# Performance work log

Hardware: AMD Instinct MI355X
Metric: run time of the kernel (lower is better)

Reference implementation:

```python
import jax, jax.numpy as jnp
import numpy as np

N_NODES = 64
KS = (52, 42, 34)  # ceil(0.8*64), ceil(0.8*52), ceil(0.8*42)


def _gcn(x, A, W, b):
    # GCNConv(improved=True): self-loop fill 2.0, symmetric normalization. A[tgt, src], weighted.
    n = A.shape[0]
    Ah = A + 2.0 * jnp.eye(n, dtype=A.dtype)
    d = Ah.sum(-1)
    dis = jnp.where(d > 0, jax.lax.rsqrt(d), 0.0)
    An = dis[:, None] * Ah * dis[None, :]
    return An @ (x @ W) + b


def _augment(A):
    # GraphUNet.augment_adj: add self loops (weight 1), A2 = A1 @ A1, remove self loops
    n = A.shape[0]
    eye = jnp.eye(n, dtype=A.dtype)
    A1 = A + eye
    return (A1 @ A1) * (1.0 - eye)


def _pool(x, A, w, k):
    # TopKPooling: score = tanh(x.w/||w||), keep top-k, scale kept features by score
    s = jnp.tanh((x @ w) / jnp.linalg.norm(w))
    sv, perm = jax.lax.top_k(s, k)
    return x[perm] * sv[:, None], A[perm][:, perm], perm


def _unet(x, A, dw0, db0, dws, dbs, pws, uws, ubs, uwl, ubl):
    # GraphUNet(depth=3, sum_res=True), single graph: x [n, F2], A [n, n]
    x = jax.nn.relu(_gcn(x, A, dw0, db0))
    xs, As, perms = [x], [A], []
    for i in range(3):
        A = _augment(A)
        x, A, perm = _pool(x, A, pws[i], KS[i])
        x = jax.nn.relu(_gcn(x, A, dws[i], dbs[i]))
        if i < 2:
            xs.append(x)
            As.append(A)
        perms.append(perm)
    for i in range(3):
        j = 2 - i
        res, Aj, perm = xs[j], As[j], perms[j]
        x = res + jnp.zeros_like(res).at[perm].set(x)
        if i < 2:
            x = jax.nn.relu(_gcn(x, Aj, uws[i], ubs[i]))
        else:
            x = _gcn(x, Aj, uwl, ubl)
    return x


def _nnconv(x, src, dst, ea, mw, mb, rw, bias):
    # NNConv(aggr='mean'): per-edge MLP weight, gather-matmul-scatter-mean + root + bias
    B, E = src.shape
    fin, fout = rw.shape
    We = jax.nn.relu(ea @ mw + mb).reshape(B, E, fin, fout)  # [B,E,fin,fout]
    xs = jnp.take_along_axis(x, src[..., None], axis=1)      # [B,E,fin]
    msg = jnp.einsum('bei,beio->beo', xs, We)                # [B,E,fout]
    seg = jax.vmap(lambda m, d: jax.ops.segment_sum(m, d, num_segments=N_NODES))
    sums = seg(msg, dst)
    cnt = seg(jnp.ones(msg.shape[:2] + (1,), msg.dtype), dst)
    agg = sums / jnp.maximum(cnt, 1.0)
    return agg + x @ rw + bias


def _adj(src, dst):
    A = jnp.zeros((N_NODES, N_NODES), jnp.float32).at[dst, src].set(1.0)
    return A * (1.0 - jnp.eye(N_NODES, dtype=jnp.float32))


def _branch(x, ei, ea, mlp1, mlp2, u1, u2):
    src, dst = ei[:, 0], ei[:, 1]
    A = jax.vmap(_adj)(src, dst)
    x = jax.nn.relu(_nnconv(x, src, dst, ea, *mlp1))
    x = jax.nn.relu(jax.vmap(lambda h, a: _unet(h, a, *u1))(x, A))
    x = jax.nn.relu(_nnconv(x, src, dst, ea, *mlp2))
    x = jax.nn.relu(jax.vmap(lambda h, a: _unet(h, a, *u2))(x, A))
    return x.mean(axis=1)  # global_mean_pool (equal-sized graphs)


def setup_inputs() -> dict:
    key = jax.random.key(0)
    keys = iter(jax.random.split(key, 64))
    def nrm(shape, s=1.0):
        return jax.random.normal(next(keys), shape, jnp.float32) * s
    B, n, E, F, F2, Q, H, C = 128, 64, 512, 64, 32, 16, 256, 50
    inp = {}
    inp['x1'] = nrm((B, n, F))
    inp['ei1'] = jax.random.randint(next(keys), (B, 2, E), 0, n, jnp.int32)
    inp['ea1'] = jax.random.uniform(next(keys), (B, E, 1), jnp.float32)
    inp['jw1'] = nrm((B, Q))
    inp['x2'] = nrm((B, n, F))
    inp['ei2'] = jax.random.randint(next(keys), (B, 2, E), 0, n, jnp.int32)
    inp['ea2'] = jax.random.uniform(next(keys), (B, E, 1), jnp.float32)
    inp['jw2'] = nrm((B, Q))
    inp['m1w'] = nrm((1, F * F2), 0.1)
    inp['m1b'] = nrm((F * F2,), 0.1)
    inp['r1w'] = nrm((F, F2), 0.1)
    inp['c1b'] = nrm((F2,), 0.1)
    inp['m2w'] = nrm((1, F2 * F2), 0.1)
    inp['m2b'] = nrm((F2 * F2,), 0.1)
    inp['r2w'] = nrm((F2, F2), 0.1)
    inp['c2b'] = nrm((F2,), 0.1)
    for p in ('u1', 'u2'):
        inp[p + '_dw0'] = nrm((F2, C), 0.1)
        inp[p + '_db0'] = nrm((C,), 0.1)
        inp[p + '_dws'] = nrm((3, C, C), 0.1)
        inp[p + '_dbs'] = nrm((3, C), 0.1)
        inp[p + '_pws'] = nrm((3, C), 0.1)
        inp[p + '_uws'] = nrm((2, C, C), 0.1)
        inp[p + '_ubs'] = nrm((2, C), 0.1)
        inp[p + '_uwl'] = nrm((C, F2), 0.1)
        inp[p + '_ubl'] = nrm((F2,), 0.1)
    inp['bb_w'] = nrm(((F2 + Q) * 2, H), 0.1)
    inp['bb_b'] = nrm((H,), 0.1)
    return inp


def reference(x1, ei1, ea1, jw1, x2, ei2, ea2, jw2,
              m1w, m1b, r1w, c1b, m2w, m2b, r2w, c2b,
              u1_dw0, u1_db0, u1_dws, u1_dbs, u1_pws, u1_uws, u1_ubs, u1_uwl, u1_ubl,
              u2_dw0, u2_db0, u2_dws, u2_dbs, u2_pws, u2_uws, u2_ubs, u2_uwl, u2_ubl,
              bb_w, bb_b):
    mlp1 = (m1w, m1b, r1w, c1b)
    mlp2 = (m2w, m2b, r2w, c2b)
    u1 = (u1_dw0, u1_db0, u1_dws, u1_dbs, u1_pws, u1_uws, u1_ubs, u1_uwl, u1_ubl)
    u2 = (u2_dw0, u2_db0, u2_dws, u2_dbs, u2_pws, u2_uws, u2_ubs, u2_uwl, u2_ubl)
    r1 = _branch(x1, ei1, ea1, mlp1, mlp2, u1, u2)
    r2 = _branch(x2, ei2, ea2, mlp1, mlp2, u1, u2)
    c = jnp.concatenate([r1, jw1, r2, jw2], axis=1)  # [(F2+Q)*2]
    return jax.nn.relu(c @ bb_w + bb_b)
```

## Files before the change

kernel.cpp:

```cpp
#include <hip/hip_runtime.h>
#include <math.h>

#define UT 1024
#define XS 52
#define ASTR 65

__device__ __forceinline__ float wred16(float v) {
    v += __shfl_xor(v, 8); v += __shfl_xor(v, 4);
    v += __shfl_xor(v, 2); v += __shfl_xor(v, 1);
    return v;
}

__device__ __forceinline__ void gcn_u(int n, int cin, int cout,
    float* __restrict__ x, float* __restrict__ tmp,
    const float* __restrict__ A, float* __restrict__ Wl,
    float* __restrict__ dis,
    const float* __restrict__ Wg, const float* __restrict__ bg, bool relu)
{
    const int tid = threadIdx.x;
    const int nso = (cout + 3) >> 2;
    for (int idx = tid; idx < 51 * 52; idx += UT) {
        int r = idx / 52, c = idx - r * 52;
        float v = 0.f;
        if (r < cin && c < cout) v = Wg[r * cout + c];
        else if (r == 50 && c < cout) v = bg[c];
        Wl[idx] = v;
    }
    {
        int r = tid >> 4, l = tid & 15;
        float s = 0.f;
        if (r < n) for (int j = l; j < n; j += 16) s += A[r * ASTR + j];
        s = wred16(s);
        if (l == 0 && r < n) dis[r] = 1.0f / sqrtf(2.0f + s);
    }
    __syncthreads();
    const int items = n * nso;
    for (int it = tid; it < items; it += UT) {
        int i = it / nso, o0 = (it - i * nso) * 4;
        float a0=0,a1=0,a2=0,a3=0, b0=0,b1=0,b2=0,b3=0;
        for (int k = 0; k < cin; k += 2) {
            float4 w0 = *(const float4*)&Wl[k * 52 + o0];
            float4 w1 = *(const float4*)&Wl[(k + 1) * 52 + o0];
            float x0 = x[i * XS + k], x1 = x[i * XS + k + 1];
            a0 = fmaf(x0, w0.x, a0); a1 = fmaf(x0, w0.y, a1);
            a2 = fmaf(x0, w0.z, a2); a3 = fmaf(x0, w0.w, a3);
            b0 = fmaf(x1, w1.x, b0); b1 = fmaf(x1, w1.y, b1);
            b2 = fmaf(x1, w1.z, b2); b3 = fmaf(x1, w1.w, b3);
        }
        float d = dis[i];
        float4 t;
        t.x = (a0 + b0) * d; t.y = (a1 + b1) * d;
        t.z = (a2 + b2) * d; t.w = (a3 + b3) * d;
        *(float4*)&tmp[i * XS + o0] = t;
    }
    __syncthreads();
    for (int it = tid; it < items; it += UT) {
        int i = it / nso, o0 = (it - i * nso) * 4;
        float a0=0,a1=0,a2=0,a3=0, b0=0,b1=0,b2=0,b3=0;
        for (int j = 0; j < n; j += 2) {
            float4 t0 = *(const float4*)&tmp[j * XS + o0];
            float4 t1 = *(const float4*)&tmp[(j + 1) * XS + o0];
            float av0 = A[i * ASTR + j], av1 = A[i * ASTR + j + 1];
            a0 = fmaf(av0, t0.x, a0); a1 = fmaf(av0, t0.y, a1);
            a2 = fmaf(av0, t0.z, a2); a3 = fmaf(av0, t0.w, a3);
            b0 = fmaf(av1, t1.x, b0); b1 = fmaf(av1, t1.y, b1);
            b2 = fmaf(av1, t1.z, b2); b3 = fmaf(av1, t1.w, b3);
        }
        float4 bias = *(const float4*)&Wl[50 * 52 + o0];
        float4 s0 = *(const float4*)&tmp[i * XS + o0];
        float d = dis[i];
        float4 r;
        r.x = fmaf(d, (a0 + b0) + 2.f * s0.x, bias.x);
        r.y = fmaf(d, (a1 + b1) + 2.f * s0.y, bias.y);
        r.z = fmaf(d, (a2 + b2) + 2.f * s0.z, bias.z);
        r.w = fmaf(d, (a3 + b3) + 2.f * s0.w, bias.w);
        if (relu) {
            r.x = fmaxf(r.x, 0.f); r.y = fmaxf(r.y, 0.f);
            r.z = fmaxf(r.z, 0.f); r.w = fmaxf(r.w, 0.f);
        }
        *(float4*)&x[i * XS + o0] = r;
    }
    __syncthreads();
}

__device__ __forceinline__ void gcn_sparse(int cin, int cout,
    float* __restrict__ x, float* __restrict__ tmp,
    const int* __restrict__ csrOff, const int* __restrict__ csrCol,
    float* __restrict__ dis0, float* __restrict__ Wl,
    const float* __restrict__ Wg, const float* __restrict__ bg, bool relu)
{
    const int tid = threadIdx.x;
    const int nso = (cout + 3) >> 2;
    for (int idx = tid; idx < 51 * 52; idx += UT) {
        int r = idx / 52, c = idx - r * 52;
        float v = 0.f;
        if (r < cin && c < cout) v = Wg[r * cout + c];
        else if (r == 50 && c < cout) v = bg[c];
        Wl[idx] = v;
    }
    if (tid < 64)
        dis0[tid] = 1.0f / sqrtf(2.0f + (float)(csrOff[tid + 1] - csrOff[tid]));
    __syncthreads();
    const int items = 64 * nso;
    if (tid < items) {
        int i = tid / nso, o0 = (tid - i * nso) * 4;
        float a0=0,a1=0,a2=0,a3=0, b0=0,b1=0,b2=0,b3=0;
        for (int k = 0; k < cin; k += 2) {
            float4 w0 = *(const float4*)&Wl[k * 52 + o0];
            float4 w1 = *(const float4*)&Wl[(k + 1) * 52 + o0];
            float x0 = x[i * XS + k], x1 = x[i * XS + k + 1];
            a0 = fmaf(x0, w0.x, a0); a1 = fmaf(x0, w0.y, a1);
            a2 = fmaf(x0, w0.z, a2); a3 = fmaf(x0, w0.w, a3);
            b0 = fmaf(x1, w1.x, b0); b1 = fmaf(x1, w1.y, b1);
            b2 = fmaf(x1, w1.z, b2); b3 = fmaf(x1, w1.w, b3);
        }
        float d = dis0[i];
        float4 t;
        t.x = (a0 + b0) * d; t.y = (a1 + b1) * d;
        t.z = (a2 + b2) * d; t.w = (a3 + b3) * d;
        *(float4*)&tmp[i * XS + o0] = t;
    }
    __syncthreads();
    if (tid < items) {
        int i = tid / nso, o0 = (tid - i * nso) * 4;
        int base = csrOff[i], end = csrOff[i + 1];
        float a0 = 0.f, a1 = 0.f, a2 = 0.f, a3 = 0.f;
        for (int p = base; p < end; p++) {
            int j = csrCol[p];
            float4 t = *(const float4*)&tmp[j * XS + o0];
            a0 += t.x; a1 += t.y; a2 += t.z; a3 += t.w;
        }
        float4 bias = *(const float4*)&Wl[50 * 52 + o0];
        float4 s0 = *(const float4*)&tmp[i * XS + o0];
        float d = dis0[i];
        float4 r;
        r.x = fmaf(d, a0 + 2.f * s0.x, bias.x);
        r.y = fmaf(d, a1 + 2.f * s0.y, bias.y);
        r.z = fmaf(d, a2 + 2.f * s0.z, bias.z);
        r.w = fmaf(d, a3 + 2.f * s0.w, bias.w);
        if (relu) {
            r.x = fmaxf(r.x, 0.f); r.y = fmaxf(r.y, 0.f);
            r.z = fmaxf(r.z, 0.f); r.w = fmaxf(r.w, 0.f);
        }
        *(float4*)&x[tid / nso * XS + o0] = r;
    }
    __syncthreads();
}

__device__ __forceinline__ void down_scores(int n, const float* __restrict__ wg,
                                            const float* __restrict__ px,
                                            float* __restrict__ scr)
{
    const int tid = threadIdx.x;
    int r = tid >> 4, l = tid & 15;
    float s = 0.f, wn = 0.f;
    for (int q = l; q < 50; q += 16) {
        float wv = wg[q];
        wn = fmaf(wv, wv, wn);
        s  = fmaf(px[r * XS + q], wv, s);
    }
    s = wred16(s); wn = wred16(wn);
    if (l == 0 && r < n) scr[r] = tanhf(s / sqrtf(wn));
}

__device__ __forceinline__ void down_rest(int n, int kk,
    float* __restrict__ px, float* __restrict__ pt_,
    float* __restrict__ pA, float* __restrict__ pF,
    float* __restrict__ scr, float* __restrict__ dis, float* __restrict__ svals,
    int* __restrict__ perm, const float* __restrict__ dw,
    const float* __restrict__ db)
{
    const int tid = threadIdx.x;
    __syncthreads();
    if (tid < 64) {
        float v = (tid < n) ? scr[tid] : -2.0f;
        int id = tid;
        for (int sz = 2; sz <= 64; sz <<= 1)
            for (int st = sz >> 1; st > 0; st >>= 1) {
                float ov = __shfl_xor(v, st);
                int oi = __shfl_xor(id, st);
                bool up = ((tid & sz) == 0);
                bool lower = ((tid & st) == 0);
                bool less = (v > ov) || (v == ov && id < oi);
                bool keep = (up == lower) ? less : !less;
                if (!keep) { v = ov; id = oi; }
            }
        if (tid < kk) { perm[tid] = id; svals[tid] = v; }
    }
    __syncthreads();
    for (int idx = tid; idx < n * 13; idx += UT) {
        int m = idx / 13, u0 = (idx - (idx / 13) * 13) * 4;
        float4 gv;
        gv.x = (u0 + 0 < kk) ? pA[m * ASTR + perm[u0 + 0]] : 0.f;
        gv.y = (u0 + 1 < kk) ? pA[m * ASTR + perm[u0 + 1]] : 0.f;
        gv.z = (u0 + 2 < kk) ? pA[m * ASTR + perm[u0 + 2]] : 0.f;
        gv.w = (u0 + 3 < kk) ? pA[m * ASTR + perm[u0 + 3]] : 0.f;
        *(float4*)&pt_[m * XS + u0] = gv;
    }
    float gx0=0, gx1=0, gx2=0, gx3=0; int gdst = -1;
    if (tid < kk * 13) {
        int t = tid / 13, q0 = (tid - t * 13) * 4;
        float sv = svals[t]; int p = perm[t];
        gx0 = px[p * XS + q0 + 0] * sv; gx1 = px[p * XS + q0 + 1] * sv;
        gx2 = px[p * XS + q0 + 2] * sv; gx3 = px[p * XS + q0 + 3] * sv;
        gdst = t * XS + q0;
    }
    __syncthreads();
    if (gdst >= 0) {
        px[gdst] = gx0; px[gdst + 1] = gx1; px[gdst + 2] = gx2; px[gdst + 3] = gx3;
    }
    int nst = (kk + 3) >> 2;
    for (int it = tid; it < kk * nst; it += UT) {
        int t = it / nst, u0 = (it - t * nst) * 4;
        int p = perm[t];
        float a0=0,a1=0,a2=0,a3=0, c0=0,c1=0,c2=0,c3=0;
        for (int m = 0; m < n; m += 2) {
            float4 g0 = *(const float4*)&pt_[m * XS + u0];
            float4 g1 = *(const float4*)&pt_[(m + 1) * XS + u0];
            float q0v = pA[p * ASTR + m], q1v = pA[p * ASTR + m + 1];
            a0 = fmaf(q0v, g0.x, a0); a1 = fmaf(q0v, g0.y, a1);
            a2 = fmaf(q0v, g0.z, a2); a3 = fmaf(q0v, g0.w, a3);
            c0 = fmaf(q1v, g1.x, c0); c1 = fmaf(q1v, g1.y, c1);
            c2 = fmaf(q1v, g1.z, c2); c3 = fmaf(q1v, g1.w, c3);
        }
        float4 gg = *(const float4*)&pt_[p * XS + u0];
        float v;
        v = (a0 + c0) + 2.f * gg.x; pF[t * ASTR + u0 + 0] = (u0 + 0 == t) ? 0.f : v;
        v = (a1 + c1) + 2.f * gg.y; pF[t * ASTR + u0 + 1] = (u0 + 1 == t) ? 0.f : v;
        v = (a2 + c2) + 2.f * gg.z; pF[t * ASTR + u0 + 2] = (u0 + 2 == t) ? 0.f : v;
        v = (a3 + c3) + 2.f * gg.w; pF[t * ASTR + u0 + 3] = (u0 + 3 == t) ? 0.f : v;
    }
    __syncthreads();
    gcn_u(kk, 50, 50, px, pt_, pF, pA, dis, dw, db, true);
}

__global__ __launch_bounds__(UT)
void unet_kernel(const float* __restrict__ xin, const float* __restrict__ wsA,
                 const int* __restrict__ wsCsrO, const int* __restrict__ wsCsrC,
                 const float* __restrict__ dw0, const float* __restrict__ db0,
                 const float* __restrict__ dws, const float* __restrict__ dbs,
                 const float* __restrict__ pws,
                 const float* __restrict__ uws, const float* __restrict__ ubs,
                 const float* __restrict__ uwl, const float* __restrict__ ubl,
                 float* __restrict__ ws_xs, float* __restrict__ ws_As,
                 float* __restrict__ outp, int mean_mode)
{
    const int g = blockIdx.x, tid = threadIdx.x;
    __shared__ __align__(16) float Aa[64 * ASTR];
    __shared__ __align__(16) float Ab[64 * ASTR];
    __shared__ __align__(16) float x0c[64 * XS];
    __shared__ __align__(16) float x1c[64 * XS];
    __shared__ float scr[64];
    __shared__ float dis[64];
    __shared__ float dis0[64];
    __shared__ float svals[64];
    __shared__ int   permL[192];
    __shared__ int   csrOffL[65];
    __shared__ int   csrColL[512];

    float *pA = Aa, *pF = Ab, *px = x0c, *pt_ = x1c;
    float* xs_g = ws_xs + (size_t)g * 9984;
    float* as_g = ws_As + (size_t)g * 6144;
    const float* wsAg = wsA + (size_t)g * 4160;
    const int nsz[4] = {64, 52, 42, 34};

    {
        const float* xg = xin + (size_t)g * 2048;
        for (int idx = tid; idx < 512; idx += UT) {
            int i = idx >> 3, o0 = (idx & 7) * 4;
            *(float4*)&px[i * XS + o0] = *(const float4*)&xg[i * 32 + o0];
        }
        for (int idx = tid; idx < 4160; idx += UT) pA[idx] = wsAg[idx];
        if (tid < 65) csrOffL[tid] = wsCsrO[(size_t)g * 66 + tid];
        if (tid >= 128 && tid < 640) csrColL[tid - 128] = wsCsrC[(size_t)g * 512 + tid - 128];
    }
    __syncthreads();

    gcn_sparse(32, 50, px, pt_, csrOffL, csrColL, dis0, pF, dw0, db0, true);

    for (int lvl = 0; lvl < 3; lvl++) {
        int n = nsz[lvl], kk = nsz[lvl + 1];
        down_scores(n, pws + lvl * 50, px, scr);
        {
            float* xd = xs_g + lvl * 3328;
            for (int idx = tid; idx < 3328; idx += UT) xd[idx] = px[idx];
            if (lvl == 1) for (int idx = tid; idx < 3380; idx += UT) as_g[idx] = pA[idx];
            if (lvl == 2) for (int idx = tid; idx < 2730; idx += UT) as_g[3380 + idx] = pA[idx];
        }
        down_rest(n, kk, px, pt_, pA, pF, scr, dis, svals, permL + lvl * 64,
                  dws + lvl * 2500, dbs + lvl * 50);
        { float* t = pA; pA = pF; pF = t; }
    }

    for (int i2 = 0; i2 < 3; i2++) {
        int j = 2 - i2;
        int kc = nsz[j + 1];
        {
            const float* resg = xs_g + j * 3328;
            for (int idx = tid; idx < 3328; idx += UT) pt_[idx] = resg[idx];
            if (j == 1) {
                for (int idx = tid; idx < 3380; idx += UT) pF[idx] = as_g[idx];
            } else if (j == 2) {
                for (int idx = tid; idx < 2730; idx += UT) pF[idx] = as_g[3380 + idx];
            }
        }
        __syncthreads();
        const int* perm = permL + j * 64;
        for (int it = tid; it < kc * 13; it += UT) {
            int t = it / 13, q0 = (it - t * 13) * 4;
            int p = perm[t];
            pt_[p*XS+q0+0] += px[t*XS+q0+0]; pt_[p*XS+q0+1] += px[t*XS+q0+1];
            pt_[p*XS+q0+2] += px[t*XS+q0+2]; pt_[p*XS+q0+3] += px[t*XS+q0+3];
        }
        __syncthreads();
        if (i2 < 2)
            gcn_u(nsz[j], 50, 50, pt_, px, pF, pA, dis, uws + i2 * 2500, ubs + i2 * 50, true);
        else
            gcn_sparse(50, 32, pt_, px, csrOffL, csrColL, dis0, pF, uwl, ubl, false);
        { float* t2 = px; px = pt_; pt_ = t2; }
        { float* t2 = pA; pA = pF; pF = t2; }
    }

    if (mean_mode) {
        int r = tid >> 4, l = tid & 15;
        if (r < 32) {
            float s = 0.f;
            for (int i = l; i < 64; i += 16) s += fmaxf(px[i * XS + r], 0.f);
            s = wred16(s);
            if (l == 0) outp[(size_t)g * 32 + r] = s * (1.0f / 64.0f);
        }
    } else {
        float* og = outp + (size_t)g * 2048;
        for (int idx = tid; idx < 512; idx += UT) {
            int i = idx >> 3, o0 = (idx & 7) * 4;
            float4 vv = *(const float4*)&px[i * XS + o0];
            vv.x = fmaxf(vv.x, 0.f); vv.y = fmaxf(vv.y, 0.f);
            vv.z = fmaxf(vv.z, 0.f); vv.w = fmaxf(vv.w, 0.f);
            *(float4*)&og[i * 32 + o0] = vv;
        }
    }
}

template<int FIN>
__device__ __forceinline__ void nnconv_core(
    const float* __restrict__ xl, const float* __restrict__ rwl,
    float* __restrict__ sums,
    const int* __restrict__ sSrcL, const int* __restrict__ sDstL,
    const float* __restrict__ sEaL, const float* __restrict__ cnt,
    const float* __restrict__ mw, const float* __restrict__ mb,
    const float* __restrict__ bias, float* __restrict__ xout_g)
{
    const int tid = threadIdx.x;
    constexpr int ICN = FIN / 16;
    constexpr int EPT = 512 / (UT / (32 * ICN));
    const int o = tid & 31, ic = (tid >> 5) & (ICN - 1), er = tid / (32 * ICN);
    float mwr[16], mbr[16];
    #pragma unroll
    for (int z = 0; z < 16; z++) {
        mwr[z] = mw[(ic * 16 + z) * 32 + o];
        mbr[z] = mb[(ic * 16 + z) * 32 + o];
    }
    float xc[16];
    int sprev = -1;
    for (int e = er * EPT; e < er * EPT + EPT; e++) {
        int s = sSrcL[e];
        if (s != sprev) {
            sprev = s;
            *(float4*)&xc[0]  = *(const float4*)&xl[s * FIN + ic * 16 + 0];
            *(float4*)&xc[4]  = *(const float4*)&xl[s * FIN + ic * 16 + 4];
            *(float4*)&xc[8]  = *(const float4*)&xl[s * FIN + ic * 16 + 8];
            *(float4*)&xc[12] = *(const float4*)&xl[s * FIN + ic * 16 + 12];
        }
        float av = sEaL[e]; int d = sDstL[e];
        float ac0 = 0.f, ac1 = 0.f, ac2 = 0.f, ac3 = 0.f;
        #pragma unroll
        for (int zb = 0; zb < 16; zb += 4) {
            ac0 = fmaf(xc[zb + 0], fmaxf(fmaf(av, mwr[zb + 0], mbr[zb + 0]), 0.f), ac0);
            ac1 = fmaf(xc[zb + 1], fmaxf(fmaf(av, mwr[zb + 1], mbr[zb + 1]), 0.f), ac1);
            ac2 = fmaf(xc[zb + 2], fmaxf(fmaf(av, mwr[zb + 2], mbr[zb + 2]), 0.f), ac2);
            ac3 = fmaf(xc[zb + 3], fmaxf(fmaf(av, mwr[zb + 3], mbr[zb + 3]), 0.f), ac3);
        }
        float acc = (ac0 + ac1) + (ac2 + ac3);
        acc += __shfl_down(acc, 32);
        if ((tid & 32) == 0) atomicAdd(&sums[d * 32 + o], acc);
    }
    __syncthreads();
    {
        int nn = tid >> 4, o0 = (tid & 15) * 2;
        float a0 = 0.f, a1 = 0.f, b0 = 0.f, b1 = 0.f;
        for (int i = 0; i < FIN; i += 2) {
            float xv0 = xl[nn * FIN + i], xv1 = xl[nn * FIN + i + 1];
            float2 w0 = *(const float2*)&rwl[i * 32 + o0];
            float2 w1 = *(const float2*)&rwl[(i + 1) * 32 + o0];
            a0 = fmaf(xv0, w0.x, a0); a1 = fmaf(xv0, w0.y, a1);
            b0 = fmaf(xv1, w1.x, b0); b1 = fmaf(xv1, w1.y, b1);
        }
        float inv = 1.0f / fmaxf(cnt[nn], 1.f);
        float2 sv = *(const float2*)&sums[nn * 32 + o0];
        xout_g[nn * 32 + o0]     = fmaxf(fmaf(sv.x, inv, (a0 + b0) + bias[o0]),     0.f);
        xout_g[nn * 32 + o0 + 1] = fmaxf(fmaf(sv.y, inv, (a1 + b1) + bias[o0 + 1]), 0.f);
    }
}

__global__ __launch_bounds__(UT)
void nnconv1_kernel(const float* __restrict__ x1, const float* __restrict__ x2,
                    const int* __restrict__ ei1, const int* __restrict__ ei2,
                    const float* __restrict__ ea1, const float* __restrict__ ea2,
                    const float* __restrict__ mw, const float* __restrict__ mb,
                    const float* __restrict__ rw, const float* __restrict__ bias,
                    float* __restrict__ wsA, int* __restrict__ wsSrt,
                    int* __restrict__ wsCsrO, int* __restrict__ wsCsrC,
                    float* __restrict__ xout)
{
    const int g = blockIdx.x, tid = threadIdx.x;
    __shared__ __align__(16) float xl[4096];
    __shared__ __align__(16) float rwl[2048];
    __shared__ __align__(16) float sums[2048];
    __shared__ __align__(16) float Al[4160];
    __shared__ int   srcl[512];
    __shared__ int   dstl[512];
    __shared__ float eal[512];
    __shared__ int   sSrcL[512];
    __shared__ int   sDstL[512];
    __shared__ float sEaL[512];
    __shared__ float cnt[64];
    __shared__ int   sTot[64];
    __shared__ int   sOff[65];
    __shared__ int   rowc[64];
    __shared__ int   csrOffL[65];

    const float* xg; const int* eig; const float* eag;
    if (g < 128) {
        xg = x1 + (size_t)g * 4096; eig = ei1 + (size_t)g * 1024; eag = ea1 + (size_t)g * 512;
    } else {
        int h = g - 128;
        xg = x2 + (size_t)h * 4096; eig = ei2 + (size_t)h * 1024; eag = ea2 + (size_t)h * 512;
    }
    int* chunkCnt = (int*)sums;

    for (int i = tid; i < 4096; i += UT) xl[i] = xg[i];
    for (int e = tid; e < 512; e += UT) {
        srcl[e] = eig[e]; dstl[e] = eig[512 + e]; eal[e] = eag[e];
    }
    for (int i = tid; i < 4160; i += UT) Al[i] = 0.f;
    for (int i = tid; i < 1024; i += UT) chunkCnt[i] = 0;
    if (tid < 64) cnt[tid] = 0.f;
    __syncthreads();
    for (int e = tid; e < 512; e += UT) Al[dstl[e] * ASTR + srcl[e]] = 1.f;
    for (int e = tid; e < 512; e += UT) atomicAdd(&chunkCnt[(e >> 5) * 64 + srcl[e]], 1);
    __syncthreads();
    if (tid < 64) {
        Al[tid * ASTR + tid] = 0.f;
        int run = 0;
        for (int c = 0; c < 16; c++) {
            int t = chunkCnt[c * 64 + tid];
            chunkCnt[c * 64 + tid] = run; run += t;
        }
        sTot[tid] = run;
    }
    __syncthreads();
    if (tid < 64) {
        int v = sTot[tid]; int x = v;
        #pragma unroll
        for (int d = 1; d < 64; d <<= 1) {
            int y = __shfl_up(x, d);
            if (tid >= d) x += y;
        }
        sOff[tid] = x - v;
        if (tid == 63) sOff[64] = x;
    }
    if (tid >= 64 && tid < 128) {
        int i = tid - 64; int c = 0;
        for (int j = 0; j < 64; j++) c += (Al[i * ASTR + j] != 0.f) ? 1 : 0;
        rowc[i] = c;
    }
    for (int e = tid; e < 512; e += UT) atomicAdd(&cnt[dstl[e]], 1.f);
    for (int i = tid; i < 2048; i += UT) rwl[i] = rw[i];
    for (int i = tid; i < 4160; i += UT) wsA[(size_t)g * 4160 + i] = Al[i];
    __syncthreads();
    if (tid < 64) {
        int v = rowc[tid]; int x = v;
        #pragma unroll
        for (int d = 1; d < 64; d <<= 1) {
            int y = __shfl_up(x, d);
            if (tid >= d) x += y;
        }
        csrOffL[tid] = x - v;
        if (tid == 63) csrOffL[64] = x;
    }
    for (int e = tid; e < 512; e += UT) {
        int s = srcl[e]; int c = e >> 5; int lr = 0;
        for (int e2 = (c << 5); e2 < e; e2++) lr += (srcl[e2] == s) ? 1 : 0;
        int pos = sOff[s] + chunkCnt[c * 64 + s] + lr;
        sSrcL[pos] = s; sDstL[pos] = dstl[e]; sEaL[pos] = eal[e];
    }
    __syncthreads();
    if (tid < 64) {
        int p = csrOffL[tid];
        for (int j = 0; j < 64; j++)
            if (Al[tid * ASTR + j] != 0.f) wsCsrC[(size_t)g * 512 + (p++)] = j;
    }
    if (tid >= 64 && tid < 129) wsCsrO[(size_t)g * 66 + (tid - 64)] = csrOffL[tid - 64];
    for (int e = tid; e < 512; e += UT) {
        wsSrt[(size_t)g * 1536 + e] = sSrcL[e];
        wsSrt[(size_t)g * 1536 + 512 + e] = sDstL[e];
        ((float*)wsSrt)[(size_t)g * 1536 + 1024 + e] = sEaL[e];
    }
    for (int i = tid; i < 2048; i += UT) sums[i] = 0.f;
    __syncthreads();

    nnconv_core<64>(xl, rwl, sums, sSrcL, sDstL, sEaL, cnt, mw, mb, bias,
                    xout + (size_t)g * 2048);
}

__global__ __launch_bounds__(UT)
void nnconv2_kernel(const float* __restrict__ xin,
                    const int* __restrict__ wsSrt,
                    const float* __restrict__ mw, const float* __restrict__ mb,
                    const float* __restrict__ rw, const float* __restrict__ bias,
                    float* __restrict__ xout)
{
    const int g = blockIdx.x, tid = threadIdx.x;
    __shared__ __align__(16) float xl[2048];
    __shared__ __align__(16) float rwl[1024];
    __shared__ __align__(16) float sums[2048];
    __shared__ int   sSrcL[512];
    __shared__ int   sDstL[512];
    __shared__ float sEaL[512];
    __shared__ float cnt[64];

    const float* xg = xin + (size_t)g * 2048;
    for (int i = tid; i < 2048; i += UT) { xl[i] = xg[i]; sums[i] = 0.f; }
    for (int i = tid; i < 1024; i += UT) rwl[i] = rw[i];
    for (int e = tid; e < 512; e += UT) {
        sSrcL[e] = wsSrt[(size_t)g * 1536 + e];
        sDstL[e] = wsSrt[(size_t)g * 1536 + 512 + e];
        sEaL[e]  = ((const float*)wsSrt)[(size_t)g * 1536 + 1024 + e];
    }
    if (tid < 64) cnt[tid] = 0.f;
    __syncthreads();
    for (int e = tid; e < 512; e += UT) atomicAdd(&cnt[sDstL[e]], 1.f);
    __syncthreads();

    nnconv_core<32>(xl, rwl, sums, sSrcL, sDstL, sEaL, cnt, mw, mb, bias,
                    xout + (size_t)g * 2048);
}

__global__ __launch_bounds__(256)
void head_kernel(const float* __restrict__ r,
                 const float* __restrict__ jw1, const float* __restrict__ jw2,
                 const float* __restrict__ bw, const float* __restrict__ bb,
                 float* __restrict__ out)
{
    const int b = blockIdx.x, h = threadIdx.x;
    float acc = bb[h];
    const float* r1 = r + (size_t)b * 32;
    const float* r2 = r + (size_t)(128 + b) * 32;
    #pragma unroll
    for (int q = 0; q < 32; q++) acc += r1[q] * bw[q * 256 + h];
    #pragma unroll
    for (int q = 0; q < 16; q++) acc += jw1[b * 16 + q] * bw[(32 + q) * 256 + h];
    #pragma unroll
    for (int q = 0; q < 32; q++) acc += r2[q] * bw[(48 + q) * 256 + h];
    #pragma unroll
    for (int q = 0; q < 16; q++) acc += jw2[b * 16 + q] * bw[(80 + q) * 256 + h];
    out[(size_t)b * 256 + h] = fmaxf(acc, 0.f);
}

extern "C" void kernel_launch(void* const* d_in, const int* in_sizes, int n_in,
                              void* d_out, int out_size, void* d_ws, size_t ws_size,
                              hipStream_t stream)
{
    const float* x1  = (const float*)d_in[0];
    const int*   ei1 = (const int*)  d_in[1];
    const float* ea1 = (const float*)d_in[2];
    const float* jw1 = (const float*)d_in[3];
    const float* x2  = (const float*)d_in[4];
    const int*   ei2 = (const int*)  d_in[5];
    const float* ea2 = (const float*)d_in[6];
    const float* jw2 = (const float*)d_in[7];
    const float* m1w = (const float*)d_in[8];
    const float* m1b = (const float*)d_in[9];
    const float* r1w = (const float*)d_in[10];
    const float* c1b = (const float*)d_in[11];
    const float* m2w = (const float*)d_in[12];
    const float* m2b = (const float*)d_in[13];
    const float* r2w = (const float*)d_in[14];
    const float* c2b = (const float*)d_in[15];
    const float* u1p[9]; for (int i = 0; i < 9; i++) u1p[i] = (const float*)d_in[16 + i];
    const float* u2p[9]; for (int i = 0; i < 9; i++) u2p[i] = (const float*)d_in[25 + i];
    const float* bbw = (const float*)d_in[34];
    const float* bbb = (const float*)d_in[35];

    char* ws = (char*)d_ws;
    size_t off = 0;
    float* wsA  = (float*)(ws + off); off += 256ull * 4160 * 4;
    float* xc1  = (float*)(ws + off); off += 256ull * 2048 * 4;
    float* xu1  = (float*)(ws + off); off += 256ull * 2048 * 4;
    float* xc2  = (float*)(ws + off); off += 256ull * 2048 * 4;
    float* rr   = (float*)(ws + off); off += 256ull * 32 * 4;
    float* wxs  = (float*)(ws + off); off += 256ull * 9984 * 4;
    float* wAs  = (float*)(ws + off); off += 256ull * 6144 * 4;
    int*   wSrt = (int*)  (ws + off); off += 256ull * 1536 * 4;
    int*   wCsO = (int*)  (ws + off); off += 256ull * 66 * 4;
    int*   wCsC = (int*)  (ws + off); off += 256ull * 512 * 4;
    (void)ws_size; (void)in_sizes; (void)n_in; (void)out_size;

    nnconv1_kernel<<<256, UT, 0, stream>>>(x1, x2, ei1, ei2, ea1, ea2,
                                           m1w, m1b, r1w, c1b,
                                           wsA, wSrt, wCsO, wCsC, xc1);
    unet_kernel<<<256, UT, 0, stream>>>(xc1, wsA, wCsO, wCsC,
        u1p[0], u1p[1], u1p[2], u1p[3], u1p[4], u1p[5], u1p[6], u1p[7], u1p[8],
        wxs, wAs, xu1, 0);
    nnconv2_kernel<<<256, UT, 0, stream>>>(xu1, wSrt, m2w, m2b, r2w, c2b, xc2);
    unet_kernel<<<256, UT, 0, stream>>>(xc2, wsA, wCsO, wCsC,
        u2p[0], u2p[1], u2p[2], u2p[3], u2p[4], u2p[5], u2p[6], u2p[7], u2p[8],
        wxs, wAs, rr, 1);
    head_kernel<<<128, 256, 0, stream>>>(rr, jw1, jw2, bbw, bbb, (float*)d_out);
}
```

Baseline: 337.2 us.

## Sort NNConv edges by destination and aggregate per node without atomics

Edges are now bucketed by destination instead of source, so each wavefront owns four destination nodes and sums their messages in registers, writing the aggregate directly with no shared-memory atomics. Counts come from the CSR offsets, so the separate count pass and the dst array are removed, and a smaller edge record is passed to the second NNConv kernel. Each thread now loads the full half-feature slice per edge instead of caching per source. Per-wave work becomes uneven when in-degrees differ, and one GCN store index is also changed.

```diff
diff --git a/kernel.cpp b/kernel.cpp
--- a/kernel.cpp
+++ b/kernel.cpp
@@ -142,7 +142,7 @@
             r.x = fmaxf(r.x, 0.f); r.y = fmaxf(r.y, 0.f);
             r.z = fmaxf(r.z, 0.f); r.w = fmaxf(r.w, 0.f);
         }
-        *(float4*)&x[tid / nso * XS + o0] = r;
+        *(float4*)&x[i * XS + o0] = r;
     }
     __syncthreads();
 }
@@ -344,45 +344,40 @@
 template<int FIN>
 __device__ __forceinline__ void nnconv_core(
     const float* __restrict__ xl, const float* __restrict__ rwl,
-    float* __restrict__ sums,
-    const int* __restrict__ sSrcL, const int* __restrict__ sDstL,
-    const float* __restrict__ sEaL, const float* __restrict__ cnt,
+    float* __restrict__ agg,
+    const int* __restrict__ dOff, const int* __restrict__ sSrc,
+    const float* __restrict__ sEa,
     const float* __restrict__ mw, const float* __restrict__ mb,
     const float* __restrict__ bias, float* __restrict__ xout_g)
 {
+    constexpr int CH = FIN / 2;
     const int tid = threadIdx.x;
-    constexpr int ICN = FIN / 16;
-    constexpr int EPT = 512 / (UT / (32 * ICN));
-    const int o = tid & 31, ic = (tid >> 5) & (ICN - 1), er = tid / (32 * ICN);
-    float mwr[16], mbr[16];
+    const int o = tid & 31, ic = (tid >> 5) & 1, wv = tid >> 6;
+    float mwr[CH], mbr[CH];
     #pragma unroll
-    for (int z = 0; z < 16; z++) {
-        mwr[z] = mw[(ic * 16 + z) * 32 + o];
-        mbr[z] = mb[(ic * 16 + z) * 32 + o];
-    }
-    float xc[16];
-    int sprev = -1;
-    for (int e = er * EPT; e < er * EPT + EPT; e++) {
-        int s = sSrcL[e];
-        if (s != sprev) {
-            sprev = s;
-            *(float4*)&xc[0]  = *(const float4*)&xl[s * FIN + ic * 16 + 0];
-            *(float4*)&xc[4]  = *(const float4*)&xl[s * FIN + ic * 16 + 4];
-            *(float4*)&xc[8]  = *(const float4*)&xl[s * FIN + ic * 16 + 8];
-            *(float4*)&xc[12] = *(const float4*)&xl[s * FIN + ic * 16 + 12];
-        }
-        float av = sEaL[e]; int d = sDstL[e];
+    for (int z = 0; z < CH; z++) {
+        mwr[z] = mw[(ic * CH + z) * 32 + o];
+        mbr[z] = mb[(ic * CH + z) * 32 + o];
+    }
+    for (int dd = 0; dd < 4; dd++) {
+        int d = wv * 4 + dd;
+        int b = dOff[d], e = dOff[d + 1];
         float ac0 = 0.f, ac1 = 0.f, ac2 = 0.f, ac3 = 0.f;
-        #pragma unroll
-        for (int zb = 0; zb < 16; zb += 4) {
-            ac0 = fmaf(xc[zb + 0], fmaxf(fmaf(av, mwr[zb + 0], mbr[zb + 0]), 0.f), ac0);
-            ac1 = fmaf(xc[zb + 1], fmaxf(fmaf(av, mwr[zb + 1], mbr[zb + 1]), 0.f), ac1);
-            ac2 = fmaf(xc[zb + 2], fmaxf(fmaf(av, mwr[zb + 2], mbr[zb + 2]), 0.f), ac2);
-            ac3 = fmaf(xc[zb + 3], fmaxf(fmaf(av, mwr[zb + 3], mbr[zb + 3]), 0.f), ac3);
+        for (int p = b; p < e; p++) {
+            int s = sSrc[p];
+            float av = sEa[p];
+            #pragma unroll
+            for (int z = 0; z < CH; z += 4) {
+                float4 xv = *(const float4*)&xl[s * FIN + ic * CH + z];
+                ac0 = fmaf(xv.x, fmaxf(fmaf(av, mwr[z + 0], mbr[z + 0]), 0.f), ac0);
+                ac1 = fmaf(xv.y, fmaxf(fmaf(av, mwr[z + 1], mbr[z + 1]), 0.f), ac1);
+                ac2 = fmaf(xv.z, fmaxf(fmaf(av, mwr[z + 2], mbr[z + 2]), 0.f), ac2);
+                ac3 = fmaf(xv.w, fmaxf(fmaf(av, mwr[z + 3], mbr[z + 3]), 0.f), ac3);
+            }
         }
         float acc = (ac0 + ac1) + (ac2 + ac3);
         acc += __shfl_down(acc, 32);
-        if ((tid & 32) == 0) atomicAdd(&sums[d * 32 + o], acc);
+        if (ic == 0) agg[d * 32 + o] = acc;
     }
     __syncthreads();
     {
@@ -395,8 +390,9 @@
             a0 = fmaf(xv0, w0.x, a0); a1 = fmaf(xv0, w0.y, a1);
             b0 = fmaf(xv1, w1.x, b0); b1 = fmaf(xv1, w1.y, b1);
         }
-        float inv = 1.0f / fmaxf(cnt[nn], 1.f);
-        float2 sv = *(const float2*)&sums[nn * 32 + o0];
+        float cn  = (float)(dOff[nn + 1] - dOff[nn]);
+        float inv = 1.0f / fmaxf(cn, 1.f);
+        float2 sv = *(const float2*)&agg[nn * 32 + o0];
         xout_g[nn * 32 + o0]     = fmaxf(fmaf(sv.x, inv, (a0 + b0) + bias[o0]),     0.f);
         xout_g[nn * 32 + o0 + 1] = fmaxf(fmaf(sv.y, inv, (a1 + b1) + bias[o0 + 1]), 0.f);
     }
@@ -408,24 +404,22 @@
                     const float* __restrict__ ea1, const float* __restrict__ ea2,
                     const float* __restrict__ mw, const float* __restrict__ mb,
                     const float* __restrict__ rw, const float* __restrict__ bias,
-                    float* __restrict__ wsA, int* __restrict__ wsSrt,
+                    float* __restrict__ wsA, int* __restrict__ wsEdg,
                     int* __restrict__ wsCsrO, int* __restrict__ wsCsrC,
                     float* __restrict__ xout)
 {
     const int g = blockIdx.x, tid = threadIdx.x;
     __shared__ __align__(16) float xl[4096];
     __shared__ __align__(16) float rwl[2048];
-    __shared__ __align__(16) float sums[2048];
+    __shared__ __align__(16) float agg[2048];
     __shared__ __align__(16) float Al[4160];
     __shared__ int   srcl[512];
     __shared__ int   dstl[512];
     __shared__ float eal[512];
-    __shared__ int   sSrcL[512];
-    __shared__ int   sDstL[512];
+    __shared__ int   sSrc[512];
     __shared__ float sEaL[512];
-    __shared__ float cnt[64];
     __shared__ int   sTot[64];
-    __shared__ int   sOff[65];
+    __shared__ int   dOff[65];
     __shared__ int   rowc[64];
     __shared__ int   csrOffL[65];
 
@@ -436,18 +430,17 @@
         int h = g - 128;
         xg = x2 + (size_t)h * 4096; eig = ei2 + (size_t)h * 1024; eag = ea2 + (size_t)h * 512;
     }
-    int* chunkCnt = (int*)sums;
-
-    for (int i = tid; i < 4096; i += UT) xl[i] = xg[i];
-    for (int e = tid; e < 512; e += UT) {
-        srcl[e] = eig[e]; dstl[e] = eig[512 + e]; eal[e] = eag[e];
-    }
+    int* chunkCnt = (int*)agg;
+
+    *(float4*)&xl[tid * 4] = *(const float4*)&xg[tid * 4];
+    if (tid < 512) { srcl[tid] = eig[tid]; dstl[tid] = eig[512 + tid]; eal[tid] = eag[tid]; }
     for (int i = tid; i < 4160; i += UT) Al[i] = 0.f;
-    for (int i = tid; i < 1024; i += UT) chunkCnt[i] = 0;
-    if (tid < 64) cnt[tid] = 0.f;
-    __syncthreads();
-    for (int e = tid; e < 512; e += UT) Al[dstl[e] * ASTR + srcl[e]] = 1.f;
-    for (int e = tid; e < 512; e += UT) atomicAdd(&chunkCnt[(e >> 5) * 64 + srcl[e]], 1);
+    chunkCnt[tid] = 0;
+    __syncthreads();
+    if (tid < 512) {
+        Al[dstl[tid] * ASTR + srcl[tid]] = 1.f;
+        atomicAdd(&chunkCnt[(tid >> 5) * 64 + dstl[tid]], 1);
+    }
     __syncthreads();
     if (tid < 64) {
         Al[tid * ASTR + tid] = 0.f;
@@ -462,37 +455,36 @@
     if (tid < 64) {
         int v = sTot[tid]; int x = v;
         #pragma unroll
-        for (int d = 1; d < 64; d <<= 1) {
-            int y = __shfl_up(x, d);
-            if (tid >= d) x += y;
-        }
-        sOff[tid] = x - v;
-        if (tid == 63) sOff[64] = x;
+        for (int dl = 1; dl < 64; dl <<= 1) {
+            int y = __shfl_up(x, dl);
+            if (tid >= dl) x += y;
+        }
+        dOff[tid] = x - v;
+        if (tid == 63) dOff[64] = x;
     }
     if (tid >= 64 && tid < 128) {
         int i = tid - 64; int c = 0;
         for (int j = 0; j < 64; j++) c += (Al[i * ASTR + j] != 0.f) ? 1 : 0;
         rowc[i] = c;
     }
-    for (int e = tid; e < 512; e += UT) atomicAdd(&cnt[dstl[e]], 1.f);
     for (int i = tid; i < 2048; i += UT) rwl[i] = rw[i];
     for (int i = tid; i < 4160; i += UT) wsA[(size_t)g * 4160 + i] = Al[i];
     __syncthreads();
     if (tid < 64) {
         int v = rowc[tid]; int x = v;
         #pragma unroll
-        for (int d = 1; d < 64; d <<= 1) {
-            int y = __shfl_up(x, d);
-            if (tid >= d) x += y;
+        for (int dl = 1; dl < 64; dl <<= 1) {
+            int y = __shfl_up(x, dl);
+            if (tid >= dl) x += y;
         }
         csrOffL[tid] = x - v;
         if (tid == 63) csrOffL[64] = x;
     }
-    for (int e = tid; e < 512; e += UT) {
-        int s = srcl[e]; int c = e >> 5; int lr = 0;
-        for (int e2 = (c << 5); e2 < e; e2++) lr += (srcl[e2] == s) ? 1 : 0;
-        int pos = sOff[s] + chunkCnt[c * 64 + s] + lr;
-        sSrcL[pos] = s; sDstL[pos] = dstl[e]; sEaL[pos] = eal[e];
+    if (tid < 512) {
+        int dk = dstl[tid]; int c = tid >> 5; int lr = 0;
+        for (int e2 = (c << 5); e2 < tid; e2++) lr += (dstl[e2] == dk) ? 1 : 0;
+        int pos = dOff[dk] + chunkCnt[c * 64 + dk] + lr;
+        sSrc[pos] = srcl[tid]; sEaL[pos] = eal[tid];
     }
     __syncthreads();
     if (tid < 64) {
@@ -501,21 +493,20 @@
             if (Al[tid * ASTR + j] != 0.f) wsCsrC[(size_t)g * 512 + (p++)] = j;
     }
     if (tid >= 64 && tid < 129) wsCsrO[(size_t)g * 66 + (tid - 64)] = csrOffL[tid - 64];
-    for (int e = tid; e < 512; e += UT) {
-        wsSrt[(size_t)g * 1536 + e] = sSrcL[e];
-        wsSrt[(size_t)g * 1536 + 512 + e] = sDstL[e];
-        ((float*)wsSrt)[(size_t)g * 1536 + 1024 + e] = sEaL[e];
-    }
-    for (int i = tid; i < 2048; i += UT) sums[i] = 0.f;
-    __syncthreads();
-
-    nnconv_core<64>(xl, rwl, sums, sSrcL, sDstL, sEaL, cnt, mw, mb, bias,
+    if (tid >= 192 && tid < 257) wsEdg[(size_t)g * 1152 + (tid - 192)] = dOff[tid - 192];
+    if (tid < 512) {
+        wsEdg[(size_t)g * 1152 + 66 + tid] = sSrc[tid];
+        ((float*)wsEdg)[(size_t)g * 1152 + 578 + tid] = sEaL[tid];
+    }
+    __syncthreads();
+
+    nnconv_core<64>(xl, rwl, agg, dOff, sSrc, sEaL, mw, mb, bias,
                     xout + (size_t)g * 2048);
 }
 
 __global__ __launch_bounds__(UT)
 void nnconv2_kernel(const float* __restrict__ xin,
-                    const int* __restrict__ wsSrt,
+                    const int* __restrict__ wsEdg,
                     const float* __restrict__ mw, const float* __restrict__ mb,
                     const float* __restrict__ rw, const float* __restrict__ bias,
                     float* __restrict__ xout)
@@ -523,26 +514,22 @@
     const int g = blockIdx.x, tid = threadIdx.x;
     __shared__ __align__(16) float xl[2048];
     __shared__ __align__(16) float rwl[1024];
-    __shared__ __align__(16) float sums[2048];
-    __shared__ int   sSrcL[512];
-    __shared__ int   sDstL[512];
+    __shared__ __align__(16) float agg[2048];
+    __shared__ int   dOff[65];
+    __shared__ int   sSrc[512];
     __shared__ float sEaL[512];
-    __shared__ float cnt[64];
 
     const float* xg = xin + (size_t)g * 2048;
-    for (int i = tid; i < 2048; i += UT) { xl[i] = xg[i]; sums[i] = 0.f; }
-    for (int i = tid; i < 1024; i += UT) rwl[i] = rw[i];
-    for (int e = tid; e < 512; e += UT) {
-        sSrcL[e] = wsSrt[(size_t)g * 1536 + e];
-        sDstL[e] = wsSrt[(size_t)g * 1536 + 512 + e];
-        sEaL[e]  = ((const float*)wsSrt)[(size_t)g * 1536 + 1024 + e];
-    }
-    if (tid < 64) cnt[tid] = 0.f;
-    __syncthreads();
-    for (int e = tid; e < 512; e += UT) atomicAdd(&cnt[sDstL[e]], 1.f);
-    __syncthreads();
-
-    nnconv_core<32>(xl, rwl, sums, sSrcL, sDstL, sEaL, cnt, mw, mb, bias,
+    if (tid < 512) *(float4*)&xl[tid * 4] = *(const float4*)&xg[tid * 4];
+    if (tid < 1024) rwl[tid] = rw[tid];
+    if (tid < 65) dOff[tid] = wsEdg[(size_t)g * 1152 + tid];
+    if (tid >= 128 && tid < 640) {
+        sSrc[tid - 128] = wsEdg[(size_t)g * 1152 + 66 + (tid - 128)];
+        sEaL[tid - 128] = ((const float*)wsEdg)[(size_t)g * 1152 + 578 + (tid - 128)];
+    }
+    __syncthreads();
+
+    nnconv_core<32>(xl, rwl, agg, dOff, sSrc, sEaL, mw, mb, bias,
                     xout + (size_t)g * 2048);
 }
 
@@ -601,18 +588,18 @@
     float* rr   = (float*)(ws + off); off += 256ull * 32 * 4;
     float* wxs  = (float*)(ws + off); off += 256ull * 9984 * 4;
     float* wAs  = (float*)(ws + off); off += 256ull * 6144 * 4;
-    int*   wSrt = (int*)  (ws + off); off += 256ull * 1536 * 4;
+    int*   wEdg = (int*)  (ws + off); off += 256ull * 1152 * 4;
     int*   wCsO = (int*)  (ws + off); off += 256ull * 66 * 4;
     int*   wCsC = (int*)  (ws + off); off += 256ull * 512 * 4;
     (void)ws_size; (void)in_sizes; (void)n_in; (void)out_size;
 
     nnconv1_kernel<<<256, UT, 0, stream>>>(x1, x2, ei1, ei2, ea1, ea2,
                                            m1w, m1b, r1w, c1b,
-                                           wsA, wSrt, wCsO, wCsC, xc1);
+                                           wsA, wEdg, wCsO, wCsC, xc1);
     unet_kernel<<<256, UT, 0, stream>>>(xc1, wsA, wCsO, wCsC,
         u1p[0], u1p[1], u1p[2], u1p[3], u1p[4], u1p[5], u1p[6], u1p[7], u1p[8],
         wxs, wAs, xu1, 0);
-    nnconv2_kernel<<<256, UT, 0, stream>>>(xu1, wSrt, m2w, m2b, r2w, c2b, xc2);
+    nnconv2_kernel<<<256, UT, 0, stream>>>(xu1, wEdg, m2w, m2b, r2w, c2b, xc2);
     unet_kernel<<<256, UT, 0, stream>>>(xc2, wsA, wCsO, wCsC,
         u2p[0], u2p[1], u2p[2], u2p[3], u2p[4], u2p[5], u2p[6], u2p[7], u2p[8],
         wxs, wAs, rr, 1);
```

After: 304.0 us. -9.8%, faster.
